# Performance work log

Measured on AMD Instinct MI355X. Metric: run time of the kernel, lower is better.

## Reference

```python
import jax, jax.numpy as jnp
import numpy as np

B, C, H, W = 4, 512, 64, 64
INTER = 64  # C // channel_stride


def setup_inputs() -> dict:
    key = jax.random.key(0)
    ks = jax.random.split(key, 5)
    s = 0.02  # small init scale for numerical stability of softmax logits
    return {
        "inputs": jax.random.normal(ks[0], (B, C, H, W), dtype=jnp.float32),
        "Wq": jax.random.normal(ks[1], (INTER, C), dtype=jnp.float32) * s,
        "bq": jnp.zeros((INTER,), dtype=jnp.float32),
        "Wk": jax.random.normal(ks[2], (INTER, C), dtype=jnp.float32) * s,
        "bk": jnp.zeros((INTER,), dtype=jnp.float32),
        "Wv": jax.random.normal(ks[3], (C, C), dtype=jnp.float32) * s,
        "bv": jnp.zeros((C,), dtype=jnp.float32),
        "gamma": jax.random.normal(ks[4], (1,), dtype=jnp.float32),
    }


def reference(inputs, Wq, bq, Wk, bk, Wv, bv, gamma):
    b, c, h, w = inputs.shape
    n = h * w
    x = inputs.reshape(b, c, n)  # (B, C, N)
    # 1x1 convs == per-pixel linear projections
    q = jnp.einsum('dc,bcn->bnd', Wq, x) + bq            # (B, N, d)
    k = jnp.einsum('dc,bcn->bdn', Wk, x) + bk[:, None]   # (B, d, N)
    v = jnp.einsum('oc,bcn->bon', Wv, x) + bv[:, None]   # (B, O, N)
    # affinity: (B, Nq, Nk), softmax over keys (last dim), no scaling (as in source)
    affinity = jax.nn.softmax(jnp.einsum('bnd,bdm->bnm', q, k), axis=-1)
    # note: torch does bmm(value, affinity) -> out[b,o,m] = sum_j v[b,o,j] * A[b,j,m]
    out = jnp.einsum('bon,bnm->bom', v, affinity)        # (B, O, N)
    return gamma * out.reshape(b, -1, h, w) + inputs
```

## Files before the change

### kernel.cpp

```cpp
#include <hip/hip_runtime.h>
#include <stdint.h>

typedef __attribute__((ext_vector_type(8))) short short8;
typedef __attribute__((ext_vector_type(4))) float f32x4;
typedef __attribute__((ext_vector_type(8))) unsigned short u16x8;
typedef __attribute__((ext_vector_type(4))) unsigned short u16x4;
typedef __attribute__((ext_vector_type(2))) unsigned short u16x2;
typedef unsigned short u16;

#define NPIX 4096
#define CCH  512
#define DD   64


__device__ inline float b2f(u16 h){
  union { unsigned int i; float f; } u; u.i = ((unsigned int)h) << 16; return u.f;
}
__device__ inline u16 f2b(float f){
  union { float f; unsigned int i; } u; u.f = f;
  return (u16)((u.i + 0x7fffu + ((u.i >> 16) & 1u)) >> 16);
}
__device__ inline void gl2lds16(const void* g, void* l){
  __builtin_amdgcn_global_load_lds((const __attribute__((address_space(1))) unsigned int*)g,
                                   (__attribute__((address_space(3))) unsigned int*)l, 16, 0, 0);
}
__device__ inline f32x4 mfma16(short8 a, short8 b, f32x4 c){
  return __builtin_amdgcn_mfma_f32_16x16x32_bf16(a, b, c, 0, 0, 0);
}

__global__ __launch_bounds__(256) void k0_transpose(const float* __restrict__ x,
    u16* __restrict__ xT, const float* __restrict__ Wq, const float* __restrict__ Wk,
    const float* __restrict__ Wv, u16* __restrict__ Wqkb, u16* __restrict__ Wvb){
  if (blockIdx.z == 4){
    int bid = blockIdx.x * 8 + blockIdx.y;
    for (int r = 0; r < 3; ++r){
      int i = (r * 512 + bid) * 256 + threadIdx.x;
      if (i < 65536){
        int row = i >> 9, col = i & 511;
        float v = (row < 64) ? Wq[(row << 9) + col] : Wk[((row - 64) << 9) + col];
        Wqkb[(row << 9) + (col ^ ((row & 7) << 3))] = f2b(v);
      } else if (i < 327680){
        int j = i - 65536;
        int row = j >> 9, col = j & 511;
        Wvb[(row << 9) + (col ^ ((row & 7) << 3))] = f2b(Wv[j]);
      }
    }
    return;
  }
  __shared__ u16 tile[64][66];
  const int b = blockIdx.z;
  const int n0 = blockIdx.x * 64, c0 = blockIdx.y * 64;
  const float* xb = x + ((size_t)b * CCH + c0) * NPIX + n0;
  #pragma unroll
  for (int r = 0; r < 16; ++r){
    int id = r * 256 + threadIdx.x;
    int cc = id >> 6, nn = id & 63;
    tile[nn][cc] = f2b(xb[(size_t)cc * NPIX + nn]);
  }
  __syncthreads();
  u16* xTb = xT + ((size_t)b * NPIX + n0) * CCH + c0;
  #pragma unroll
  for (int r = 0; r < 8; ++r){
    int id = r * 256 + threadIdx.x;
    int nn = id >> 5, c2 = id & 31;
    int colp = (2 * c2) ^ ((nn & 7) << 3);
    *(u16x2*)(xTb + (size_t)nn * CCH + colp) = *(const u16x2*)&tile[nn][2 * c2];
  }
}

__global__ __launch_bounds__(256) void k1_qk(const u16* __restrict__ xT,
    const u16* __restrict__ Wqk, const float* __restrict__ bq,
    const float* __restrict__ bk, u16* __restrict__ Qb, u16* __restrict__ Kb){
  __shared__ __align__(16) u16 As[128*64];
  __shared__ __align__(16) u16 Bs[128*64];
  const int b  = blockIdx.z;
  const int n0 = blockIdx.x * 128;
  const u16* Ab = xT + ((size_t)b * NPIX + n0) * CCH;
  const int t = threadIdx.x, wave = t >> 6, lane = t & 63, q = lane >> 4, l16 = lane & 15;
  const int wr = (wave >> 1) * 64, wc = (wave & 1) * 64;
  const int sw = l16 & 7;
  f32x4 acc[4][4];
  #pragma unroll
  for (int i = 0; i < 4; ++i)
    #pragma unroll
    for (int j = 0; j < 4; ++j) acc[i][j] = (f32x4){0.f,0.f,0.f,0.f};

  for (int k0 = 0; k0 < CCH; k0 += 64){
    __syncthreads();
    #pragma unroll
    for (int r = 0; r < 4; ++r){
      int id = r * 256 + t;
      int row = id >> 3, ko = (id & 7) << 3;
      gl2lds16(Ab + (size_t)row * CCH + k0 + ko, &As[id * 8]);
      gl2lds16(Wqk + (size_t)row * CCH + k0 + ko, &Bs[id * 8]);
    }
    __syncthreads();
    #pragma unroll
    for (int s = 0; s < 2; ++s){
      const int ca = ((s*4 + q) ^ sw) << 3;
      short8 af[4], bfr[4];
      #pragma unroll
      for (int i = 0; i < 4; ++i){
        af[i]  = *(const short8*)&As[(wr + i*16 + l16)*64 + ca];
        bfr[i] = *(const short8*)&Bs[(wc + i*16 + l16)*64 + ca];
      }
      #pragma unroll
      for (int i = 0; i < 4; ++i)
        #pragma unroll
        for (int j = 0; j < 4; ++j)
          acc[i][j] = mfma16(af[i], bfr[j], acc[i][j]);
    }
  }
  #pragma unroll
  for (int i = 0; i < 4; ++i){
    #pragma unroll
    for (int j = 0; j < 4; ++j){
      int col = wc + j*16 + l16;
      #pragma unroll
      for (int r2 = 0; r2 < 4; ++r2){
        int n = n0 + wr + i*16 + q*4 + r2;
        int sw8 = (n & 7) << 3;
        float v = acc[i][j][r2];
        if (col < 64) Qb[((size_t)b * NPIX + n) * DD + (col ^ sw8)]        = f2b(v + bq[col]);
        else          Kb[((size_t)b * NPIX + n) * DD + ((col - 64) ^ sw8)] = f2b(v + bk[col - 64]);
      }
    }
  }
}

__global__ __launch_bounds__(256) void k2_v(const u16* __restrict__ xT,
    const u16* __restrict__ Wvb, const float* __restrict__ bv, u16* __restrict__ Vb){
  __shared__ __align__(16) u16 As[128*64];
  __shared__ __align__(16) u16 Bs[128*64];
  const int b  = blockIdx.z;
  const int n0 = blockIdx.x * 128;
  const int o0 = blockIdx.y * 128;
  const u16* Ab = Wvb + (size_t)o0 * CCH;
  const u16* Bb = xT + ((size_t)b * NPIX + n0) * CCH;
  const int t = threadIdx.x, wave = t >> 6, lane = t & 63, q = lane >> 4, l16 = lane & 15;
  const int wr = (wave >> 1) * 64, wc = (wave & 1) * 64;
  const int sw = l16 & 7;
  f32x4 acc[4][4];
  #pragma unroll
  for (int i = 0; i < 4; ++i)
    #pragma unroll
    for (int j = 0; j < 4; ++j) acc[i][j] = (f32x4){0.f,0.f,0.f,0.f};

  for (int k0 = 0; k0 < CCH; k0 += 64){
    __syncthreads();
    #pragma unroll
    for (int r = 0; r < 4; ++r){
      int id = r * 256 + t;
      int row = id >> 3, ko = (id & 7) << 3;
      gl2lds16(Ab + (size_t)row * CCH + k0 + ko, &As[id * 8]);
      gl2lds16(Bb + (size_t)row * CCH + k0 + ko, &Bs[id * 8]);
    }
    __syncthreads();
    #pragma unroll
    for (int s = 0; s < 2; ++s){
      const int ca = ((s*4 + q) ^ sw) << 3;
      short8 af[4], bfr[4];
      #pragma unroll
      for (int i = 0; i < 4; ++i){
        af[i]  = *(const short8*)&As[(wr + i*16 + l16)*64 + ca];
        bfr[i] = *(const short8*)&Bs[(wc + i*16 + l16)*64 + ca];
      }
      #pragma unroll
      for (int i = 0; i < 4; ++i)
        #pragma unroll
        for (int j = 0; j < 4; ++j)
          acc[i][j] = mfma16(af[i], bfr[j], acc[i][j]);
    }
  }
  #pragma unroll
  for (int i = 0; i < 4; ++i){
    #pragma unroll
    for (int j = 0; j < 4; ++j){
      int n = n0 + wc + j*16 + l16;
      #pragma unroll
      for (int r2 = 0; r2 < 4; ++r2){
        int o = o0 + wr + i*16 + q*4 + r2;
        int np = n ^ ((o & 7) << 3);
        Vb[((size_t)b * CCH + o) * NPIX + np] = f2b(acc[i][j][r2] + bv[o]);
      }
    }
  }
}

__global__ __launch_bounds__(256) void k3_logits(const u16* __restrict__ Qb,
    const u16* __restrict__ Kb, u16* __restrict__ E, float* __restrict__ Z, int b0){
  __shared__ __align__(16) u16 smem[128*136];
  u16* As = smem;
  u16* Bs = smem + 128*64;
  const int bloc = blockIdx.z, b = b0 + bloc;
  const int n0 = blockIdx.x * 128;
  const int m0 = blockIdx.y * 128;
  const u16* Ab = Kb + ((size_t)b * NPIX + m0) * DD;
  const u16* Bb = Qb + ((size_t)b * NPIX + n0) * DD;
  const int t = threadIdx.x, wave = t >> 6, lane = t & 63, q = lane >> 4, l16 = lane & 15;
  const int wr = (wave >> 1) * 64, wc = (wave & 1) * 64;
  const int sw = l16 & 7;
  f32x4 acc[4][4];
  #pragma unroll
  for (int i = 0; i < 4; ++i)
    #pragma unroll
    for (int j = 0; j < 4; ++j) acc[i][j] = (f32x4){0.f,0.f,0.f,0.f};

  #pragma unroll
  for (int r = 0; r < 4; ++r){
    int id = r * 256 + t;
    int row = id >> 3, ko = (id & 7) << 3;
    gl2lds16(Ab + row * DD + ko, &As[id * 8]);
    gl2lds16(Bb + row * DD + ko, &Bs[id * 8]);
  }
  __syncthreads();
  #pragma unroll
  for (int s = 0; s < 2; ++s){
    const int ca = ((s*4 + q) ^ sw) << 3;
    short8 af[4], bfr[4];
    #pragma unroll
    for (int i = 0; i < 4; ++i){
      af[i]  = *(const short8*)&As[(wr + i*16 + l16)*64 + ca];
      bfr[i] = *(const short8*)&Bs[(wc + i*16 + l16)*64 + ca];
    }
    #pragma unroll
    for (int i = 0; i < 4; ++i)
      #pragma unroll
      for (int j = 0; j < 4; ++j)
        acc[i][j] = mfma16(af[i], bfr[j], acc[i][j]);
  }
  __syncthreads();
  u16* tile = smem;
  float colsum[4] = {0.f, 0.f, 0.f, 0.f};
  #pragma unroll
  for (int i = 0; i < 4; ++i){
    #pragma unroll
    for (int j = 0; j < 4; ++j){
      #pragma unroll
      for (int r2 = 0; r2 < 4; ++r2){
        int mrow = wr + i*16 + q*4 + r2;
        int ncol = wc + j*16 + l16;
        float l = fminf(fmaxf(acc[i][j][r2], -60.f), 30.f);
        float e = __expf(l);
        tile[mrow * 136 + ncol] = f2b(e);
        colsum[j] += e;
      }
    }
  }
  #pragma unroll
  for (int j = 0; j < 4; ++j){
    float v = colsum[j];
    v += __shfl_xor(v, 16, 64);
    v += __shfl_xor(v, 32, 64);
    if (q == 0) atomicAdd(&Z[(size_t)b * NPIX + n0 + wc + j*16 + l16], v);
  }
  __syncthreads();
  u16* Eb = E + (size_t)bloc * NPIX * NPIX;
  #pragma unroll
  for (int r = 0; r < 8; ++r){
    int id = r * 256 + t;
    int row = id >> 4, chunk = id & 15;
    int g = chunk >> 3, c3 = chunk & 7;
    int colp = g * 64 + ((c3 ^ (row & 7)) << 3);
    *(u16x8*)(Eb + (size_t)(m0 + row) * NPIX + n0 + colp) =
        *(const u16x8*)&tile[row * 136 + chunk * 8];
  }
}

__global__ __launch_bounds__(256) void k3b_scale(u16* __restrict__ Vb,
    const float* __restrict__ Z, const float* __restrict__ gm, int b0){
  size_t i4  = ((size_t)blockIdx.x * 256 + threadIdx.x) * 4;
  size_t off = ((size_t)b0 << 21) + i4;
  int b = (int)(off >> 21);
  int o = (int)((off >> 12) & 511);
  int np = (int)(off & (NPIX - 1));
  int nl = np ^ ((o & 7) << 3);
  float g = gm[0];
  u16x4 vv = *(const u16x4*)(Vb + off);
  f32x4 zz = *(const f32x4*)(Z + ((size_t)b << 12) + nl);
  u16x4 r;
  #pragma unroll
  for (int k = 0; k < 4; ++k) r[k] = f2b(g * b2f(vv[k]) / fmaxf(zz[k], 1e-20f));
  *(u16x4*)(Vb + off) = r;
}

__global__ __launch_bounds__(512, 2) void k4_out(const u16* __restrict__ Vs,
    const u16* __restrict__ E, const float* __restrict__ xin,
    float* __restrict__ outp, int b0){
  __shared__ __align__(16) u16 smem[3*128*64 + 3*256*64];
  u16* As = smem;
  u16* Bs = smem + 3*128*64;
  const int bloc = blockIdx.z, b = b0 + bloc;
  const int m0 = blockIdx.x * 256;
  const int o0 = blockIdx.y * 128;
  const u16* Ab = Vs + ((size_t)b * CCH + o0) * NPIX;
  const u16* Bb = E + (size_t)bloc * NPIX * NPIX + (size_t)m0 * NPIX;
  const int t = threadIdx.x, wave = t >> 6, lane = t & 63, q = lane >> 4, l16 = lane & 15;
  const int grp = wave >> 2;
  const int br  = (wave & 3) * 64;
  const int sw = l16 & 7;
  const int ca = ((grp * 4 + q) ^ sw) << 3;

  auto stageA = [&](int kt, int bi){
    const int k0 = kt << 6;
    u16* dst = As + bi * (128*64);
    #pragma unroll
    for (int r = 0; r < 2; ++r){
      int id = r * 512 + t;
      gl2lds16(Ab + (size_t)(id >> 3) * NPIX + (k0 + ((id & 7) << 3)), dst + id * 8);
    }
  };
  auto stageB = [&](int kt, int bi){
    const int k0 = kt << 6;
    u16* dst = Bs + bi * (256*64);
    #pragma unroll
    for (int r = 0; r < 4; ++r){
      int id = r * 512 + t;
      gl2lds16(Bb + (size_t)(id >> 3) * NPIX + (k0 + ((id & 7) << 3)), dst + id * 8);
    }
  };

  f32x4 acc[8][4];
  #pragma unroll
  for (int i = 0; i < 8; ++i)
    #pragma unroll
    for (int j = 0; j < 4; ++j) acc[i][j] = (f32x4){0.f,0.f,0.f,0.f};

  stageA(0, 0); stageB(0, 0);
  stageA(1, 1); stageB(1, 1);
  asm volatile("s_waitcnt vmcnt(6)" ::: "memory");
  __builtin_amdgcn_sched_barrier(0);
  __builtin_amdgcn_s_barrier();

  int bi = 0;
  for (int kt = 0; kt < NPIX / 64; ++kt){
    const int bi2 = (bi >= 1) ? bi - 1 : 2;
    const bool pf = (kt + 2) < NPIX / 64;
    const u16* Ap = As + bi * (128*64);
    const u16* Bp = Bs + bi * (256*64);
    short8 af[8], bfr[4];
    #pragma unroll
    for (int i = 0; i < 8; ++i) af[i]  = *(const short8*)&Ap[(i*16 + l16)*64 + ca];
    #pragma unroll
    for (int j = 0; j < 4; ++j) bfr[j] = *(const short8*)&Bp[(br + j*16 + l16)*64 + ca];
    if (pf){ stageA(kt + 2, bi2); stageB(kt + 2, bi2); }
    asm volatile("s_waitcnt lgkmcnt(0)" ::: "memory");
    __builtin_amdgcn_sched_barrier(0);
    __builtin_amdgcn_s_setprio(1);
    #pragma unroll
    for (int i = 0; i < 8; ++i)
      #pragma unroll
      for (int j = 0; j < 4; ++j)
        acc[i][j] = mfma16(af[i], bfr[j], acc[i][j]);
    __builtin_amdgcn_s_setprio(0);
    if (pf){ asm volatile("s_waitcnt vmcnt(6)" ::: "memory"); }
    else   { asm volatile("s_waitcnt vmcnt(0)" ::: "memory"); }
    __builtin_amdgcn_sched_barrier(0);
    __builtin_amdgcn_s_barrier();
    bi = (bi == 2) ? 0 : bi + 1;
  }

  float* red = (float*)smem;
  if (grp == 1){
    #pragma unroll
    for (int i = 0; i < 8; ++i)
      #pragma unroll
      for (int j = 0; j < 4; ++j)
        *(f32x4*)&red[(size_t)(br + j*16 + l16) * 132 + i*16 + q*4] = acc[i][j];
  }
  __syncthreads();
  if (grp == 0){
    const float* xb = xin + (size_t)b * CCH * NPIX;
    float* ob = outp + (size_t)b * CCH * NPIX;
    #pragma unroll
    for (int i = 0; i < 8; ++i){
      #pragma unroll
      for (int j = 0; j < 4; ++j){
        f32x4 p = *(const f32x4*)&red[(size_t)(br + j*16 + l16) * 132 + i*16 + q*4];
        int m = m0 + br + j*16 + l16;
        #pragma unroll
        for (int r2 = 0; r2 < 4; ++r2){
          int o = o0 + i*16 + q*4 + r2;
          size_t idx = (size_t)o * NPIX + m;
          ob[idx] = acc[i][j][r2] + p[r2] + xb[idx];
        }
      }
    }
  }
}

extern "C" void kernel_launch(void* const* d_in, const int* in_sizes, int n_in,
                              void* d_out, int out_size, void* d_ws, size_t ws_size,
                              hipStream_t stream){
  (void)in_sizes; (void)n_in; (void)out_size;
  const float* x  = (const float*)d_in[0];
  const float* Wq = (const float*)d_in[1];
  const float* bq = (const float*)d_in[2];
  const float* Wk = (const float*)d_in[3];
  const float* bk = (const float*)d_in[4];
  const float* Wv = (const float*)d_in[5];
  const float* bv = (const float*)d_in[6];
  const float* gm = (const float*)d_in[7];
  float* outp = (float*)d_out;

  char* ws = (char*)d_ws;
  u16*  Qb   = (u16*)(ws + 0);
  u16*  Kb   = (u16*)(ws + 2097152);
  u16*  Vb   = (u16*)(ws + 4194304);
  float* Z   = (float*)(ws + 20971520);
  u16*  Wqkb = (u16*)(ws + 21037056);
  u16*  Wvb  = (u16*)(ws + 21168128);
  u16*  xT   = (u16*)(ws + 21692416);
  u16*  E    = (u16*)(ws + 21692416);

  const size_t ebytes = (size_t)NPIX * NPIX * 2;
  const size_t base   = 21692416;
  if (ws_size < base + ebytes){
    return;
  }
  int NB = 1;
  if (ws_size >= base + 4 * ebytes) NB = 4;
  else if (ws_size >= base + 2 * ebytes) NB = 2;

  hipMemsetAsync(Z, 0, (size_t)4 * NPIX * sizeof(float), stream);
  k0_transpose<<<dim3(64, 8, 5), 256, 0, stream>>>(x, xT, Wq, Wk, Wv, Wqkb, Wvb);
  k1_qk<<<dim3(32, 1, 4), 256, 0, stream>>>(xT, Wqkb, bq, bk, Qb, Kb);
  k2_v<<<dim3(32, 4, 4), 256, 0, stream>>>(xT, Wvb, bv, Vb);
  for (int b0 = 0; b0 < 4; b0 += NB){
    int nb = NB; if (b0 + nb > 4) nb = 4 - b0;
    k3_logits<<<dim3(32, 32, nb), 256, 0, stream>>>(Qb, Kb, E, Z, b0);
    k3b_scale<<<dim3(nb * 2048), 256, 0, stream>>>(Vb, Z, gm, b0);
    k4_out<<<dim3(16, 4, nb), 512, 0, stream>>>(Vb, E, x, outp, b0);
  }
}
```

Baseline: 232.3 us.

## Load k4_out B fragments directly from global into registers, bypassing LDS

In the output GEMM, the softmax-weight operand (E) is no longer staged through shared memory. Each wave reads its own B fragments straight from global memory into registers, prefetching one k-tile ahead. This is possible because each B element is consumed by only one wave. The A operand pipeline drops from triple to double buffering, and shared memory is resized to fit the epilogue reduction buffer. The aim is to remove LDS write/read traffic and shrink the LDS footprint, at the cost of less coalesced global loads and a shorter prefetch distance for B.

```diff
diff --git a/kernel.cpp b/kernel.cpp
--- a/kernel.cpp
+++ b/kernel.cpp
@@ -287,9 +287,8 @@
 __global__ __launch_bounds__(512, 2) void k4_out(const u16* __restrict__ Vs,
     const u16* __restrict__ E, const float* __restrict__ xin,
     float* __restrict__ outp, int b0){
-  __shared__ __align__(16) u16 smem[3*128*64 + 3*256*64];
+  __shared__ __align__(16) u16 smem[67584];
   u16* As = smem;
-  u16* Bs = smem + 3*128*64;
   const int bloc = blockIdx.z, b = b0 + bloc;
   const int m0 = blockIdx.x * 256;
   const int o0 = blockIdx.y * 128;
@@ -300,6 +299,7 @@
   const int br  = (wave & 3) * 64;
   const int sw = l16 & 7;
   const int ca = ((grp * 4 + q) ^ sw) << 3;
+  const u16* bp = Bb + (size_t)(br + l16) * NPIX + (size_t)ca;
 
   auto stageA = [&](int kt, int bi){
     const int k0 = kt << 6;
@@ -310,15 +310,6 @@
       gl2lds16(Ab + (size_t)(id >> 3) * NPIX + (k0 + ((id & 7) << 3)), dst + id * 8);
     }
   };
-  auto stageB = [&](int kt, int bi){
-    const int k0 = kt << 6;
-    u16* dst = Bs + bi * (256*64);
-    #pragma unroll
-    for (int r = 0; r < 4; ++r){
-      int id = r * 512 + t;
-      gl2lds16(Bb + (size_t)(id >> 3) * NPIX + (k0 + ((id & 7) << 3)), dst + id * 8);
-    }
-  };
 
   f32x4 acc[8][4];
   #pragma unroll
@@ -326,24 +317,23 @@
     #pragma unroll
     for (int j = 0; j < 4; ++j) acc[i][j] = (f32x4){0.f,0.f,0.f,0.f};
 
-  stageA(0, 0); stageB(0, 0);
-  stageA(1, 1); stageB(1, 1);
-  asm volatile("s_waitcnt vmcnt(6)" ::: "memory");
+  short8 bfr[4];
+  stageA(0, 0);
+  #pragma unroll
+  for (int j = 0; j < 4; ++j)
+    bfr[j] = *(const short8*)(bp + (size_t)j * 16 * NPIX);
+  asm volatile("s_waitcnt vmcnt(0)" ::: "memory");
   __builtin_amdgcn_sched_barrier(0);
   __builtin_amdgcn_s_barrier();
 
-  int bi = 0;
   for (int kt = 0; kt < NPIX / 64; ++kt){
-    const int bi2 = (bi >= 1) ? bi - 1 : 2;
-    const bool pf = (kt + 2) < NPIX / 64;
+    const int bi = kt & 1;
+    const bool pf = (kt + 1) < NPIX / 64;
     const u16* Ap = As + bi * (128*64);
-    const u16* Bp = Bs + bi * (256*64);
-    short8 af[8], bfr[4];
-    #pragma unroll
-    for (int i = 0; i < 8; ++i) af[i]  = *(const short8*)&Ap[(i*16 + l16)*64 + ca];
-    #pragma unroll
-    for (int j = 0; j < 4; ++j) bfr[j] = *(const short8*)&Bp[(br + j*16 + l16)*64 + ca];
-    if (pf){ stageA(kt + 2, bi2); stageB(kt + 2, bi2); }
+    short8 af[8];
+    #pragma unroll
+    for (int i = 0; i < 8; ++i) af[i] = *(const short8*)&Ap[(i*16 + l16)*64 + ca];
+    if (pf) stageA(kt + 1, bi ^ 1);
     asm volatile("s_waitcnt lgkmcnt(0)" ::: "memory");
     __builtin_amdgcn_sched_barrier(0);
     __builtin_amdgcn_s_setprio(1);
@@ -353,11 +343,17 @@
       for (int j = 0; j < 4; ++j)
         acc[i][j] = mfma16(af[i], bfr[j], acc[i][j]);
     __builtin_amdgcn_s_setprio(0);
-    if (pf){ asm volatile("s_waitcnt vmcnt(6)" ::: "memory"); }
-    else   { asm volatile("s_waitcnt vmcnt(0)" ::: "memory"); }
+    __builtin_amdgcn_sched_barrier(0);
+    if (pf){
+      #pragma unroll
+      for (int j = 0; j < 4; ++j)
+        bfr[j] = *(const short8*)(bp + (size_t)j * 16 * NPIX + ((kt + 1) << 6));
+      asm volatile("s_waitcnt vmcnt(4)" ::: "memory");
+    } else {
+      asm volatile("s_waitcnt vmcnt(0)" ::: "memory");
+    }
     __builtin_amdgcn_sched_barrier(0);
     __builtin_amdgcn_s_barrier();
-    bi = (bi == 2) ? 0 : bi + 1;
   }
 
   float* red = (float*)smem;
```

New measurement: 244.0 us. 1.05x slower.

## Fuse softmax-normalization scaling into V projection epilogue by reordering kernels

Applied to the files above, without the earlier changes.

When the workspace is large enough, E is placed after xT so the V projection can run after the logits kernel. The V projection epilogue then multiplies by gamma/Z per pixel, which removes the separate k3b_scale pass over V. This needs a larger workspace. Otherwise it falls back to the old batched path.

```diff
diff --git a/kernel.cpp b/kernel.cpp
--- a/kernel.cpp
+++ b/kernel.cpp
@@ -129,7 +129,8 @@
 }
 
 __global__ __launch_bounds__(256) void k2_v(const u16* __restrict__ xT,
-    const u16* __restrict__ Wvb, const float* __restrict__ bv, u16* __restrict__ Vb){
+    const u16* __restrict__ Wvb, const float* __restrict__ bv, u16* __restrict__ Vb,
+    const float* __restrict__ Z, const float* __restrict__ gm, int fused){
   __shared__ __align__(16) u16 As[128*64];
   __shared__ __align__(16) u16 Bs[128*64];
   const int b  = blockIdx.z;
@@ -172,6 +173,17 @@
           acc[i][j] = mfma16(af[i], bfr[j], acc[i][j]);
     }
   }
+  float zs[4];
+  #pragma unroll
+  for (int j = 0; j < 4; ++j) zs[j] = 1.f;
+  if (fused){
+    float g = gm[0];
+    #pragma unroll
+    for (int j = 0; j < 4; ++j){
+      int n = n0 + wc + j*16 + l16;
+      zs[j] = g / fmaxf(Z[(size_t)b * NPIX + n], 1e-20f);
+    }
+  }
   #pragma unroll
   for (int i = 0; i < 4; ++i){
     #pragma unroll
@@ -181,7 +193,9 @@
       for (int r2 = 0; r2 < 4; ++r2){
         int o = o0 + wr + i*16 + q*4 + r2;
         int np = n ^ ((o & 7) << 3);
-        Vb[((size_t)b * CCH + o) * NPIX + np] = f2b(acc[i][j][r2] + bv[o]);
+        float v = acc[i][j][r2] + bv[o];
+        if (fused) v *= zs[j];
+        Vb[((size_t)b * CCH + o) * NPIX + np] = f2b(v);
       }
     }
   }
@@ -411,25 +425,34 @@
   u16*  Wqkb = (u16*)(ws + 21037056);
   u16*  Wvb  = (u16*)(ws + 21168128);
   u16*  xT   = (u16*)(ws + 21692416);
-  u16*  E    = (u16*)(ws + 21692416);
 
   const size_t ebytes = (size_t)NPIX * NPIX * 2;
   const size_t base   = 21692416;
+  const size_t xT_end = base + (size_t)4 * NPIX * CCH * 2;
   if (ws_size < base + ebytes){
     return;
   }
-  int NB = 1;
-  if (ws_size >= base + 4 * ebytes) NB = 4;
-  else if (ws_size >= base + 2 * ebytes) NB = 2;
 
   hipMemsetAsync(Z, 0, (size_t)4 * NPIX * sizeof(float), stream);
   k0_transpose<<<dim3(64, 8, 5), 256, 0, stream>>>(x, xT, Wq, Wk, Wv, Wqkb, Wvb);
   k1_qk<<<dim3(32, 1, 4), 256, 0, stream>>>(xT, Wqkb, bq, bk, Qb, Kb);
-  k2_v<<<dim3(32, 4, 4), 256, 0, stream>>>(xT, Wvb, bv, Vb);
-  for (int b0 = 0; b0 < 4; b0 += NB){
-    int nb = NB; if (b0 + nb > 4) nb = 4 - b0;
-    k3_logits<<<dim3(32, 32, nb), 256, 0, stream>>>(Qb, Kb, E, Z, b0);
-    k3b_scale<<<dim3(nb * 2048), 256, 0, stream>>>(Vb, Z, gm, b0);
-    k4_out<<<dim3(16, 4, nb), 512, 0, stream>>>(Vb, E, x, outp, b0);
-  }
-}
+
+  if (ws_size >= xT_end + 4 * ebytes){
+    u16* E = (u16*)(ws + xT_end);
+    k3_logits<<<dim3(32, 32, 4), 256, 0, stream>>>(Qb, Kb, E, Z, 0);
+    k2_v<<<dim3(32, 4, 4), 256, 0, stream>>>(xT, Wvb, bv, Vb, Z, gm, 1);
+    k4_out<<<dim3(16, 4, 4), 512, 0, stream>>>(Vb, E, x, outp, 0);
+  } else {
+    u16* E = (u16*)(ws + base);
+    int NB = 1;
+    if (ws_size >= base + 4 * ebytes) NB = 4;
+    else if (ws_size >= base + 2 * ebytes) NB = 2;
+    k2_v<<<dim3(32, 4, 4), 256, 0, stream>>>(xT, Wvb, bv, Vb, Z, gm, 0);
+    for (int b0 = 0; b0 < 4; b0 += NB){
+      int nb = NB; if (b0 + nb > 4) nb = 4 - b0;
+      k3_logits<<<dim3(32, 32, nb), 256, 0, stream>>>(Qb, Kb, E, Z, b0);
+      k3b_scale<<<dim3(nb * 2048), 256, 0, stream>>>(Vb, Z, gm, b0);
+      k4_out<<<dim3(16, 4, nb), 512, 0, stream>>>(Vb, E, x, outp, b0);
+    }
+  }
+}
```

Measured after the change: 228.0 us. No clear change (-1.8%).
